# Kernel optimization log

Measured on AMD Instinct MI355X. Metric: run time of the kernel, lower is better.

## Reference

```python
import jax, jax.numpy as jnp
import numpy as np

NODE = 100   # sensors per graph
BATCH = 64
DIM = 128    # embed dim == gnn out channels
IN_DIM = 5
TOPK = 30
INTER = 256  # out_layer hidden
EPS = 1e-5   # BatchNorm eps
SLOPE = 0.2  # leaky relu negative slope


def setup_inputs() -> dict:
    key = jax.random.key(0)
    ks = jax.random.split(key, 16)
    d = {
        "x": jax.random.normal(ks[0], (BATCH * NODE, IN_DIM), jnp.float32),
        "emb": jax.random.normal(ks[1], (NODE, DIM), jnp.float32) * 0.1,
        "w_lin": jax.random.normal(ks[2], (DIM, IN_DIM), jnp.float32) * (1.0 / np.sqrt(IN_DIM)),
        "att_i": jax.random.normal(ks[3], (DIM,), jnp.float32) * (1.0 / np.sqrt(DIM)),
        "att_j": jax.random.normal(ks[4], (DIM,), jnp.float32) * (1.0 / np.sqrt(DIM)),
        "att_em_i": jax.random.normal(ks[5], (DIM,), jnp.float32) * (1.0 / np.sqrt(DIM)),
        "att_em_j": jax.random.normal(ks[6], (DIM,), jnp.float32) * (1.0 / np.sqrt(DIM)),
        "g_bias": jax.random.normal(ks[7], (DIM,), jnp.float32) * 0.02,
        "bn1_g": jnp.ones((DIM,), jnp.float32),
        "bn1_b": jnp.zeros((DIM,), jnp.float32),
        "bn2_g": jnp.ones((DIM,), jnp.float32),
        "bn2_b": jnp.zeros((DIM,), jnp.float32),
        "bn3_g": jnp.ones((INTER,), jnp.float32),
        "bn3_b": jnp.zeros((INTER,), jnp.float32),
        "w1": jax.random.normal(ks[8], (INTER, DIM), jnp.float32) * (1.0 / np.sqrt(DIM)),
        "b1": jnp.zeros((INTER,), jnp.float32),
        "w2": jax.random.normal(ks[9], (1, INTER), jnp.float32) * (1.0 / np.sqrt(INTER)),
        "b2": jnp.zeros((1,), jnp.float32),
        "topk": TOPK,
    }
    return d


def _bn(z, g, b, axes):
    # BatchNorm1d in training mode: biased batch stats per channel (last axis)
    mu = z.mean(axes, keepdims=True)
    var = z.var(axes, keepdims=True)
    return (z - mu) / jnp.sqrt(var + EPS) * g + b


def reference(x, emb, w_lin, att_i, att_j, att_em_i, att_em_j, g_bias,
              bn1_g, bn1_b, bn2_g, bn2_b, bn3_g, bn3_b, w1, b1, w2, b2, topk):
    n, d = emb.shape
    nb = x.shape[0]            # batch*node rows
    bsz = nb // n

    # --- learned graph from cosine similarity of (detached) embeddings ---
    w = jax.lax.stop_gradient(emb)
    nrm = jnp.linalg.norm(w, axis=-1)
    cos = (w @ w.T) / (nrm[:, None] * nrm[None, :])
    _, idx = jax.lax.top_k(cos, topk)              # [n, k] neighbors j per target i
    src = idx.reshape(-1)                          # gated_j (source)
    dst = jnp.repeat(jnp.arange(n), topk)          # gated_i (target)
    off = (jnp.arange(bsz) * n)[:, None]
    src_b = (src[None, :] + off).reshape(-1)       # [bsz*n*k]
    dst_b = (dst[None, :] + off).reshape(-1)

    # --- GraphLayer: lin + gather + edge attention + segment softmax + scatter-add ---
    h = x @ w_lin.T                                # [nb, d]
    x_i = h[dst_b]
    x_j = h[src_b]
    emb_i = emb[dst_b % n]                         # all_embeddings repeated per batch
    emb_j = emb[src_b % n]
    alpha = x_i @ att_i + emb_i @ att_em_i + x_j @ att_j + emb_j @ att_em_j  # [E]
    alpha = jnp.where(alpha > 0, alpha, SLOPE * alpha)
    # segment softmax keyed by target node
    m = jax.ops.segment_max(alpha, dst_b, num_segments=nb)
    a = jnp.exp(alpha - m[dst_b])
    s = jax.ops.segment_sum(a, dst_b, num_segments=nb)
    attw = a / (s[dst_b] + 1e-16)
    agg = jax.ops.segment_sum(x_j * attw[:, None], dst_b, num_segments=nb) + g_bias

    # GNNLayer: BN + ReLU
    y = jax.nn.relu(_bn(agg, bn1_g, bn1_b, 0))     # [nb, d]

    # --- GDN head ---
    x3 = y.reshape(bsz, n, d) * emb[None]          # mul with node embeddings
    x3 = jax.nn.relu(_bn(x3, bn2_g, bn2_b, (0, 1)))
    # OutLayer: Linear -> BN -> ReLU -> Linear
    o = x3 @ w1.T + b1                             # [bsz, n, INTER]
    o = jax.nn.relu(_bn(o, bn3_g, bn3_b, (0, 1)))
    o = o @ w2.T + b2                              # [bsz, n, 1]
    return o.reshape(-1, 1)
```

## Files before the change

### kernel.cpp

```cpp
#include <hip/hip_runtime.h>

#define NODE 100
#define BATCH 64
#define DIM 128
#define IN_DIM 5
#define TOPK 30
#define INTER 256
#define NB (BATCH*NODE)
#define EPS 1e-5f
#define SLOPE 0.2f

__global__ __launch_bounds__(128) void k_lin_att(
        const float* __restrict__ x, const float* __restrict__ emb,
        const float* __restrict__ w_lin,
        const float* __restrict__ att_i, const float* __restrict__ att_j,
        const float* __restrict__ att_em_i, const float* __restrict__ att_em_j,
        float* __restrict__ h, float* __restrict__ ai, float* __restrict__ aj) {
    int row = blockIdx.x;
    int d = threadIdx.x;
    int node = row % NODE;
    float xv[IN_DIM];
#pragma unroll
    for (int c = 0; c < IN_DIM; ++c) xv[c] = x[row*IN_DIM + c];
    float hv = 0.f;
#pragma unroll
    for (int c = 0; c < IN_DIM; ++c) hv += xv[c] * w_lin[d*IN_DIM + c];
    h[row*DIM + d] = hv;
    float e = emb[node*DIM + d];
    float si = hv*att_i[d] + e*att_em_i[d];
    float sj = hv*att_j[d] + e*att_em_j[d];
    __shared__ float s1[DIM], s2[DIM];
    s1[d] = si; s2[d] = sj;
    __syncthreads();
    for (int off = 64; off > 0; off >>= 1) {
        if (d < off) { s1[d] += s1[d+off]; s2[d] += s2[d+off]; }
        __syncthreads();
    }
    if (d == 0) { ai[row] = s1[0]; aj[row] = s2[0]; }
}

__global__ __launch_bounds__(128) void k_topk(const float* __restrict__ emb,
                                              int* __restrict__ idx) {
    int i = blockIdx.x;
    int t = threadIdx.x;
    __shared__ float ei[DIM];
    __shared__ float cosv[NODE];
    __shared__ float rv[128];
    __shared__ int   ri[128];
    ei[t] = emb[i*DIM + t];
    __syncthreads();
    float ni = 0.f;
#pragma unroll
    for (int dd = 0; dd < DIM; ++dd) ni += ei[dd]*ei[dd];
    if (t < NODE) {
        float s = 0.f, nj = 0.f;
        for (int dd = 0; dd < DIM; ++dd) {
            float e = emb[t*DIM + dd];
            s += ei[dd]*e;
            nj += e*e;
        }
        cosv[t] = s / (sqrtf(ni) * sqrtf(nj));
    }
    __syncthreads();
    for (int r = 0; r < TOPK; ++r) {
        float v = (t < NODE) ? cosv[t] : -INFINITY;
        rv[t] = v; ri[t] = t;
        __syncthreads();
        for (int off = 64; off > 0; off >>= 1) {
            if (t < off) {
                float v2 = rv[t+off]; int i2 = ri[t+off];
                if (v2 > rv[t] || (v2 == rv[t] && i2 < ri[t])) { rv[t] = v2; ri[t] = i2; }
            }
            __syncthreads();
        }
        if (t == 0) {
            idx[i*TOPK + r] = ri[0];
            cosv[ri[0]] = -INFINITY;
        }
        __syncthreads();
    }
}

__global__ __launch_bounds__(128) void k_attagg(
        const float* __restrict__ h, const float* __restrict__ ai,
        const float* __restrict__ aj, const int* __restrict__ idx,
        const float* __restrict__ g_bias, float* __restrict__ agg) {
    int tgt = blockIdx.x;
    int t = threadIdx.x;
    int node = tgt % NODE;
    int base = (tgt / NODE) * NODE;
    __shared__ float w[TOPK];
    __shared__ int   srcs[TOPK];
    if (t < TOPK) {
        int s = base + idx[node*TOPK + t];
        srcs[t] = s;
        float a = ai[tgt] + aj[s];
        a = (a > 0.f) ? a : SLOPE*a;
        w[t] = a;
    }
    __syncthreads();
    if (t == 0) {
        float m = -INFINITY;
        for (int r = 0; r < TOPK; ++r) m = fmaxf(m, w[r]);
        float s = 0.f;
        for (int r = 0; r < TOPK; ++r) { float e = expf(w[r]-m); w[r] = e; s += e; }
        float inv = 1.f/(s + 1e-16f);
        for (int r = 0; r < TOPK; ++r) w[r] *= inv;
    }
    __syncthreads();
    float acc = 0.f;
#pragma unroll 5
    for (int r = 0; r < TOPK; ++r) {
        acc += w[r] * h[srcs[r]*DIM + t];
    }
    agg[tgt*DIM + t] = acc + g_bias[t];
}

__global__ __launch_bounds__(256) void k_stats(const float* __restrict__ src, int C,
                                               float* __restrict__ mu,
                                               float* __restrict__ rs) {
    int c = blockIdx.x;
    int t = threadIdx.x;
    float s = 0.f, s2 = 0.f;
    for (int r = t; r < NB; r += 256) {
        float v = src[r*C + c];
        s += v; s2 += v*v;
    }
    __shared__ float a1[256], a2[256];
    a1[t] = s; a2[t] = s2;
    __syncthreads();
    for (int off = 128; off > 0; off >>= 1) {
        if (t < off) { a1[t] += a1[t+off]; a2[t] += a2[t+off]; }
        __syncthreads();
    }
    if (t == 0) {
        float m = a1[0] / (float)NB;
        float var = a2[0]/(float)NB - m*m;
        mu[c] = m;
        rs[c] = rsqrtf(var + EPS);
    }
}

__global__ __launch_bounds__(256) void k_x3(
        const float* __restrict__ agg, const float* __restrict__ emb,
        const float* __restrict__ mu1, const float* __restrict__ rs1,
        const float* __restrict__ g1, const float* __restrict__ b1,
        float* __restrict__ x3) {
    int i = blockIdx.x*256 + threadIdx.x;
    if (i >= NB*DIM) return;
    int d = i & (DIM-1);
    int row = i >> 7;
    int node = row % NODE;
    float v = (agg[i] - mu1[d]) * rs1[d] * g1[d] + b1[d];
    v = fmaxf(v, 0.f);
    x3[i] = v * emb[node*DIM + d];
}

__global__ __launch_bounds__(256) void k_gemm1(
        const float* __restrict__ x3,
        const float* __restrict__ mu2, const float* __restrict__ rs2,
        const float* __restrict__ g2, const float* __restrict__ b2v,
        const float* __restrict__ w1, const float* __restrict__ b1v,
        float* __restrict__ o1) {
    __shared__ float aT[32][36];
    __shared__ float wT[32][260];
    int tid = threadIdx.x;
    int r0 = blockIdx.x * 32;
    int cg = tid & 63;
    int rg = tid >> 6;
    float acc[8][4];
#pragma unroll
    for (int a = 0; a < 8; ++a)
#pragma unroll
        for (int b = 0; b < 4; ++b) acc[a][b] = 0.f;

    for (int k0 = 0; k0 < DIM; k0 += 32) {
#pragma unroll
        for (int j = 0; j < 4; ++j) {
            int i = tid + j*256;
            int kk = i & 31, row = i >> 5;
            int k = k0 + kk;
            float v = (x3[(r0+row)*DIM + k] - mu2[k]) * rs2[k] * g2[k] + b2v[k];
            aT[row][kk] = fmaxf(v, 0.f);
        }
#pragma unroll
        for (int j = 0; j < 32; ++j) {
            int i = tid + j*256;
            int kk = i & 31, c = i >> 5;
            wT[kk][c] = w1[c*DIM + k0 + kk];
        }
        __syncthreads();
#pragma unroll
        for (int q4 = 0; q4 < 8; ++q4) {
            float4 av[8], wv[4];
#pragma unroll
            for (int rr = 0; rr < 8; ++rr)
                av[rr] = *(const float4*)&aT[rg*8+rr][q4*4];
#pragma unroll
            for (int q = 0; q < 4; ++q)
                wv[q] = *(const float4*)&wT[q4*4+q][cg*4];
#pragma unroll
            for (int rr = 0; rr < 8; ++rr) {
                acc[rr][0] += av[rr].x*wv[0].x + av[rr].y*wv[1].x + av[rr].z*wv[2].x + av[rr].w*wv[3].x;
                acc[rr][1] += av[rr].x*wv[0].y + av[rr].y*wv[1].y + av[rr].z*wv[2].y + av[rr].w*wv[3].y;
                acc[rr][2] += av[rr].x*wv[0].z + av[rr].y*wv[1].z + av[rr].z*wv[2].z + av[rr].w*wv[3].z;
                acc[rr][3] += av[rr].x*wv[0].w + av[rr].y*wv[1].w + av[rr].z*wv[2].w + av[rr].w*wv[3].w;
            }
        }
        __syncthreads();
    }
    int cbase = cg*4;
    float4 bv = *(const float4*)&b1v[cbase];
#pragma unroll
    for (int rr = 0; rr < 8; ++rr) {
        int row = r0 + rg*8 + rr;
        float4 o;
        o.x = acc[rr][0] + bv.x;
        o.y = acc[rr][1] + bv.y;
        o.z = acc[rr][2] + bv.z;
        o.w = acc[rr][3] + bv.w;
        *(float4*)&o1[row*INTER + cbase] = o;
    }
}

__global__ __launch_bounds__(256) void k_out(
        const float* __restrict__ o1,
        const float* __restrict__ mu3, const float* __restrict__ rs3,
        const float* __restrict__ g3, const float* __restrict__ b3,
        const float* __restrict__ w2, const float* __restrict__ b2s,
        float* __restrict__ out) {
    int row = blockIdx.x;
    int c = threadIdx.x;
    float v = (o1[row*INTER + c] - mu3[c]) * rs3[c] * g3[c] + b3[c];
    v = fmaxf(v, 0.f);
    v *= w2[c];
    __shared__ float red[256];
    red[c] = v;
    __syncthreads();
    for (int off = 128; off > 0; off >>= 1) {
        if (c < off) red[c] += red[c+off];
        __syncthreads();
    }
    if (c == 0) out[row] = red[0] + b2s[0];
}

extern "C" void kernel_launch(void* const* d_in, const int* in_sizes, int n_in,
                              void* d_out, int out_size, void* d_ws, size_t ws_size,
                              hipStream_t stream) {
    const float* x        = (const float*)d_in[0];
    const float* emb      = (const float*)d_in[1];
    const float* w_lin    = (const float*)d_in[2];
    const float* att_i    = (const float*)d_in[3];
    const float* att_j    = (const float*)d_in[4];
    const float* att_em_i = (const float*)d_in[5];
    const float* att_em_j = (const float*)d_in[6];
    const float* g_bias   = (const float*)d_in[7];
    const float* bn1_g    = (const float*)d_in[8];
    const float* bn1_b    = (const float*)d_in[9];
    const float* bn2_g    = (const float*)d_in[10];
    const float* bn2_b    = (const float*)d_in[11];
    const float* bn3_g    = (const float*)d_in[12];
    const float* bn3_b    = (const float*)d_in[13];
    const float* w1       = (const float*)d_in[14];
    const float* b1       = (const float*)d_in[15];
    const float* w2       = (const float*)d_in[16];
    const float* b2       = (const float*)d_in[17];
    float* out = (float*)d_out;

    float* ws  = (float*)d_ws;
    float* h   = ws;
    float* agg = ws + 819200;
    float* x3  = ws + 1638400;
    float* o1  = ws + 2457600;
    float* ai  = ws + 4096000;
    float* aj  = ws + 4102400;
    float* mu1 = ws + 4108800;
    float* rs1 = mu1 + 128;
    float* mu2 = rs1 + 128;
    float* rs2 = mu2 + 128;
    float* mu3 = rs2 + 128;
    float* rs3 = mu3 + 256;
    int*   idx = (int*)(ws + 4110000);

    k_lin_att<<<NB, 128, 0, stream>>>(x, emb, w_lin, att_i, att_j, att_em_i,
                                      att_em_j, h, ai, aj);
    k_topk<<<NODE, 128, 0, stream>>>(emb, idx);
    k_attagg<<<NB, 128, 0, stream>>>(h, ai, aj, idx, g_bias, agg);
    k_stats<<<DIM, 256, 0, stream>>>(agg, DIM, mu1, rs1);
    k_x3<<<(NB*DIM + 255)/256, 256, 0, stream>>>(agg, emb, mu1, rs1, bn1_g, bn1_b, x3);
    k_stats<<<DIM, 256, 0, stream>>>(x3, DIM, mu2, rs2);
    k_gemm1<<<NB/32, 256, 0, stream>>>(x3, mu2, rs2, bn2_g, bn2_b, w1, b1, o1);
    k_stats<<<INTER, 256, 0, stream>>>(o1, INTER, mu3, rs3);
    k_out<<<NB, 256, 0, stream>>>(o1, mu3, rs3, bn3_g, bn3_b, w2, b2, out);
}
```

Measured before the change: 201.9 us.

## Fuse BN statistics into producers via atomics and use wave-level reductions

New measurement: 223.3 us. +10.6%, slower.

```diff
diff --git a/kernel.cpp b/kernel.cpp
--- a/kernel.cpp
+++ b/kernel.cpp
@@ -10,184 +10,206 @@
 #define EPS 1e-5f
 #define SLOPE 0.2f
 
-__global__ __launch_bounds__(128) void k_lin_att(
+#define LIN_BLOCKS 1600
+#define TOPK_BLOCKS 25
+#define ZERO_BLOCK (LIN_BLOCKS + TOPK_BLOCKS)
+#define FRONT_GRID (ZERO_BLOCK + 1)
+
+
+__global__ __launch_bounds__(256) void k_front(
         const float* __restrict__ x, const float* __restrict__ emb,
         const float* __restrict__ w_lin,
         const float* __restrict__ att_i, const float* __restrict__ att_j,
         const float* __restrict__ att_em_i, const float* __restrict__ att_em_j,
-        float* __restrict__ h, float* __restrict__ ai, float* __restrict__ aj) {
-    int row = blockIdx.x;
-    int d = threadIdx.x;
-    int node = row % NODE;
-    float xv[IN_DIM];
-#pragma unroll
-    for (int c = 0; c < IN_DIM; ++c) xv[c] = x[row*IN_DIM + c];
-    float hv = 0.f;
-#pragma unroll
-    for (int c = 0; c < IN_DIM; ++c) hv += xv[c] * w_lin[d*IN_DIM + c];
-    h[row*DIM + d] = hv;
-    float e = emb[node*DIM + d];
-    float si = hv*att_i[d] + e*att_em_i[d];
-    float sj = hv*att_j[d] + e*att_em_j[d];
-    __shared__ float s1[DIM], s2[DIM];
-    s1[d] = si; s2[d] = sj;
-    __syncthreads();
-    for (int off = 64; off > 0; off >>= 1) {
-        if (d < off) { s1[d] += s1[d+off]; s2[d] += s2[d+off]; }
+        float* __restrict__ h, float* __restrict__ ai, float* __restrict__ aj,
+        int* __restrict__ idx, float* __restrict__ stats) {
+    int b = blockIdx.x;
+    int t = threadIdx.x;
+    int w = t >> 6;
+    int l = t & 63;
+    if (b < LIN_BLOCKS) {
+        int row = b*4 + w;
+        int node = row % NODE;
+        float xv[IN_DIM];
+#pragma unroll
+        for (int c = 0; c < IN_DIM; ++c) xv[c] = x[row*IN_DIM + c];
+        float h0 = 0.f, h1 = 0.f;
+#pragma unroll
+        for (int c = 0; c < IN_DIM; ++c) {
+            h0 += xv[c] * w_lin[l*IN_DIM + c];
+            h1 += xv[c] * w_lin[(l+64)*IN_DIM + c];
+        }
+        h[row*DIM + l]      = h0;
+        h[row*DIM + l + 64] = h1;
+        float e0 = emb[node*DIM + l], e1 = emb[node*DIM + l + 64];
+        float si = h0*att_i[l] + e0*att_em_i[l] + h1*att_i[l+64] + e1*att_em_i[l+64];
+        float sj = h0*att_j[l] + e0*att_em_j[l] + h1*att_j[l+64] + e1*att_em_j[l+64];
+#pragma unroll
+        for (int m = 32; m >= 1; m >>= 1) {
+            si += __shfl_xor(si, m, 64);
+            sj += __shfl_xor(sj, m, 64);
+        }
+        if (l == 0) { ai[row] = si; aj[row] = sj; }
+    } else if (b < ZERO_BLOCK) {
+        __shared__ float eis[4][DIM];
+        int i = (b - LIN_BLOCKS)*4 + w;
+        eis[w][l]      = emb[i*DIM + l];
+        eis[w][l + 64] = emb[i*DIM + l + 64];
         __syncthreads();
-    }
-    if (d == 0) { ai[row] = s1[0]; aj[row] = s2[0]; }
-}
-
-__global__ __launch_bounds__(128) void k_topk(const float* __restrict__ emb,
-                                              int* __restrict__ idx) {
-    int i = blockIdx.x;
-    int t = threadIdx.x;
-    __shared__ float ei[DIM];
-    __shared__ float cosv[NODE];
-    __shared__ float rv[128];
-    __shared__ int   ri[128];
-    ei[t] = emb[i*DIM + t];
-    __syncthreads();
-    float ni = 0.f;
-#pragma unroll
-    for (int dd = 0; dd < DIM; ++dd) ni += ei[dd]*ei[dd];
-    if (t < NODE) {
-        float s = 0.f, nj = 0.f;
+        int j0 = l, j1 = 64 + l;
+        bool v1ok = (j1 < NODE);
+        float d0 = 0.f, d1 = 0.f, ni = 0.f, n0 = 0.f, n1 = 0.f;
         for (int dd = 0; dd < DIM; ++dd) {
-            float e = emb[t*DIM + dd];
-            s += ei[dd]*e;
-            nj += e*e;
-        }
-        cosv[t] = s / (sqrtf(ni) * sqrtf(nj));
-    }
-    __syncthreads();
-    for (int r = 0; r < TOPK; ++r) {
-        float v = (t < NODE) ? cosv[t] : -INFINITY;
-        rv[t] = v; ri[t] = t;
-        __syncthreads();
-        for (int off = 64; off > 0; off >>= 1) {
-            if (t < off) {
-                float v2 = rv[t+off]; int i2 = ri[t+off];
-                if (v2 > rv[t] || (v2 == rv[t] && i2 < ri[t])) { rv[t] = v2; ri[t] = i2; }
+            float e = eis[w][dd];
+            ni += e*e;
+            float a0 = emb[j0*DIM + dd];
+            d0 += e*a0; n0 += a0*a0;
+            if (v1ok) { float a1 = emb[j1*DIM + dd]; d1 += e*a1; n1 += a1*a1; }
+        }
+        float sni = sqrtf(ni);
+        float c0 = d0 / (sni * sqrtf(n0));
+        float c1 = v1ok ? d1 / (sni * sqrtf(n1)) : -INFINITY;
+        for (int r = 0; r < TOPK; ++r) {
+            float bv; int bi;
+            if (c1 > c0) { bv = c1; bi = j1; } else { bv = c0; bi = j0; }
+#pragma unroll
+            for (int m = 32; m >= 1; m >>= 1) {
+                float ov = __shfl_xor(bv, m, 64);
+                int   oi = __shfl_xor(bi, m, 64);
+                if (ov > bv || (ov == bv && oi < bi)) { bv = ov; bi = oi; }
             }
-            __syncthreads();
-        }
-        if (t == 0) {
-            idx[i*TOPK + r] = ri[0];
-            cosv[ri[0]] = -INFINITY;
-        }
-        __syncthreads();
-    }
-}
-
-__global__ __launch_bounds__(128) void k_attagg(
+            if (l == 0) idx[i*TOPK + r] = bi;
+            if (bi == j0) c0 = -INFINITY;
+            if (bi == j1) c1 = -INFINITY;
+        }
+    } else {
+#pragma unroll
+        for (int q = 0; q < 4; ++q) stats[t + q*256] = 0.f;
+    }
+}
+
+__global__ __launch_bounds__(256) void k_attagg(
         const float* __restrict__ h, const float* __restrict__ ai,
         const float* __restrict__ aj, const int* __restrict__ idx,
-        const float* __restrict__ g_bias, float* __restrict__ agg) {
-    int tgt = blockIdx.x;
-    int t = threadIdx.x;
+        const float* __restrict__ g_bias, float* __restrict__ agg,
+        float* __restrict__ stats) {
+    __shared__ float sv[4][DIM], sq[4][DIM];
+    int t = threadIdx.x, w = t >> 6, l = t & 63;
+    int tgt = blockIdx.x*4 + w;
     int node = tgt % NODE;
-    int base = (tgt / NODE) * NODE;
-    __shared__ float w[TOPK];
-    __shared__ int   srcs[TOPK];
-    if (t < TOPK) {
-        int s = base + idx[node*TOPK + t];
-        srcs[t] = s;
-        float a = ai[tgt] + aj[s];
-        a = (a > 0.f) ? a : SLOPE*a;
-        w[t] = a;
-    }
+    int base = tgt - node;
+    float a = -INFINITY; int s = 0;
+    if (l < TOPK) {
+        s = base + idx[node*TOPK + l];
+        float v = ai[tgt] + aj[s];
+        a = (v > 0.f) ? v : SLOPE*v;
+    }
+    float m = a;
+#pragma unroll
+    for (int mm = 32; mm >= 1; mm >>= 1) m = fmaxf(m, __shfl_xor(m, mm, 64));
+    float e = (l < TOPK) ? expf(a - m) : 0.f;
+    float sum = e;
+#pragma unroll
+    for (int mm = 32; mm >= 1; mm >>= 1) sum += __shfl_xor(sum, mm, 64);
+    float wgt = e / (sum + 1e-16f);
+    float acc0 = 0.f, acc1 = 0.f;
+#pragma unroll 10
+    for (int r = 0; r < TOPK; ++r) {
+        float wr = __shfl(wgt, r, 64);
+        int   sr = __shfl(s,   r, 64);
+        acc0 += wr * h[sr*DIM + l];
+        acc1 += wr * h[sr*DIM + l + 64];
+    }
+    float v0 = acc0 + g_bias[l];
+    float v1 = acc1 + g_bias[l + 64];
+    agg[tgt*DIM + l]      = v0;
+    agg[tgt*DIM + l + 64] = v1;
+    sv[w][l] = v0;      sv[w][l+64] = v1;
+    sq[w][l] = v0*v0;   sq[w][l+64] = v1*v1;
     __syncthreads();
-    if (t == 0) {
-        float m = -INFINITY;
-        for (int r = 0; r < TOPK; ++r) m = fmaxf(m, w[r]);
-        float s = 0.f;
-        for (int r = 0; r < TOPK; ++r) { float e = expf(w[r]-m); w[r] = e; s += e; }
-        float inv = 1.f/(s + 1e-16f);
-        for (int r = 0; r < TOPK; ++r) w[r] *= inv;
-    }
-    __syncthreads();
-    float acc = 0.f;
-#pragma unroll 5
-    for (int r = 0; r < TOPK; ++r) {
-        acc += w[r] * h[srcs[r]*DIM + t];
-    }
-    agg[tgt*DIM + t] = acc + g_bias[t];
-}
-
-__global__ __launch_bounds__(256) void k_stats(const float* __restrict__ src, int C,
-                                               float* __restrict__ mu,
-                                               float* __restrict__ rs) {
-    int c = blockIdx.x;
-    int t = threadIdx.x;
-    float s = 0.f, s2 = 0.f;
-    for (int r = t; r < NB; r += 256) {
-        float v = src[r*C + c];
-        s += v; s2 += v*v;
-    }
-    __shared__ float a1[256], a2[256];
-    a1[t] = s; a2[t] = s2;
-    __syncthreads();
-    for (int off = 128; off > 0; off >>= 1) {
-        if (t < off) { a1[t] += a1[t+off]; a2[t] += a2[t+off]; }
-        __syncthreads();
-    }
-    if (t == 0) {
-        float m = a1[0] / (float)NB;
-        float var = a2[0]/(float)NB - m*m;
-        mu[c] = m;
-        rs[c] = rsqrtf(var + EPS);
+    if (t < DIM) {
+        float s1 = sv[0][t] + sv[1][t] + sv[2][t] + sv[3][t];
+        float s2 = sq[0][t] + sq[1][t] + sq[2][t] + sq[3][t];
+        atomicAdd(&stats[t], s1);
+        atomicAdd(&stats[DIM + t], s2);
     }
 }
 
 __global__ __launch_bounds__(256) void k_x3(
         const float* __restrict__ agg, const float* __restrict__ emb,
-        const float* __restrict__ mu1, const float* __restrict__ rs1,
         const float* __restrict__ g1, const float* __restrict__ b1,
-        float* __restrict__ x3) {
-    int i = blockIdx.x*256 + threadIdx.x;
-    if (i >= NB*DIM) return;
-    int d = i & (DIM-1);
-    int row = i >> 7;
+        float* __restrict__ stats, float* __restrict__ x3) {
+    __shared__ float pv[8][DIM], pq[8][DIM];
+    int t = threadIdx.x;
+    int i4 = blockIdx.x*256 + t;
+    int c4 = (i4 & 31) * 4;
+    int row = i4 >> 5;
     int node = row % NODE;
-    float v = (agg[i] - mu1[d]) * rs1[d] * g1[d] + b1[d];
-    v = fmaxf(v, 0.f);
-    x3[i] = v * emb[node*DIM + d];
+    float4 av = ((const float4*)agg)[i4];
+    float4 ev = *(const float4*)&emb[node*DIM + c4];
+    const float inv = 1.f/(float)NB;
+    float o[4];
+#pragma unroll
+    for (int q = 0; q < 4; ++q) {
+        int c = c4 + q;
+        float mu = stats[c] * inv;
+        float var = stats[DIM + c]*inv - mu*mu;
+        float rs = rsqrtf(var + EPS);
+        float val = (((const float*)&av)[q] - mu)*rs*g1[c] + b1[c];
+        val = fmaxf(val, 0.f);
+        o[q] = val * ((const float*)&ev)[q];
+    }
+    ((float4*)x3)[i4] = make_float4(o[0], o[1], o[2], o[3]);
+    int lr = t >> 5;
+    *(float4*)&pv[lr][c4] = make_float4(o[0], o[1], o[2], o[3]);
+    *(float4*)&pq[lr][c4] = make_float4(o[0]*o[0], o[1]*o[1], o[2]*o[2], o[3]*o[3]);
+    __syncthreads();
+    if (t < DIM) {
+        float s1 = 0.f, s2 = 0.f;
+#pragma unroll
+        for (int r = 0; r < 8; ++r) { s1 += pv[r][t]; s2 += pq[r][t]; }
+        atomicAdd(&stats[2*DIM + t], s1);
+        atomicAdd(&stats[3*DIM + t], s2);
+    }
 }
 
 __global__ __launch_bounds__(256) void k_gemm1(
         const float* __restrict__ x3,
-        const float* __restrict__ mu2, const float* __restrict__ rs2,
         const float* __restrict__ g2, const float* __restrict__ b2v,
         const float* __restrict__ w1, const float* __restrict__ b1v,
-        float* __restrict__ o1) {
+        float* __restrict__ stats, float* __restrict__ o1) {
     __shared__ float aT[32][36];
     __shared__ float wT[32][260];
+    __shared__ float ps[4][INTER], ps2[4][INTER];
     int tid = threadIdx.x;
     int r0 = blockIdx.x * 32;
     int cg = tid & 63;
     int rg = tid >> 6;
+    const float inv = 1.f/(float)NB;
     float acc[8][4];
 #pragma unroll
     for (int a = 0; a < 8; ++a)
 #pragma unroll
         for (int b = 0; b < 4; ++b) acc[a][b] = 0.f;
 
+    int kk = tid & 31;
     for (int k0 = 0; k0 < DIM; k0 += 32) {
+        int k = k0 + kk;
+        float mu = stats[2*DIM + k] * inv;
+        float var = stats[3*DIM + k]*inv - mu*mu;
+        float rs = rsqrtf(var + EPS);
+        float gg = g2[k], bb = b2v[k];
 #pragma unroll
         for (int j = 0; j < 4; ++j) {
-            int i = tid + j*256;
-            int kk = i & 31, row = i >> 5;
-            int k = k0 + kk;
-            float v = (x3[(r0+row)*DIM + k] - mu2[k]) * rs2[k] * g2[k] + b2v[k];
+            int row = (tid >> 5) + j*8;
+            float v = (x3[(r0+row)*DIM + k] - mu)*rs*gg + bb;
             aT[row][kk] = fmaxf(v, 0.f);
         }
 #pragma unroll
         for (int j = 0; j < 32; ++j) {
             int i = tid + j*256;
-            int kk = i & 31, c = i >> 5;
-            wT[kk][c] = w1[c*DIM + k0 + kk];
+            int kk2 = i & 31, c = i >> 5;
+            wT[kk2][c] = w1[c*DIM + k0 + kk2];
         }
         __syncthreads();
 #pragma unroll
@@ -211,37 +233,55 @@
     }
     int cbase = cg*4;
     float4 bv = *(const float4*)&b1v[cbase];
+    float lv[4]  = {0.f, 0.f, 0.f, 0.f};
+    float lv2[4] = {0.f, 0.f, 0.f, 0.f};
 #pragma unroll
     for (int rr = 0; rr < 8; ++rr) {
         int row = r0 + rg*8 + rr;
-        float4 o;
-        o.x = acc[rr][0] + bv.x;
-        o.y = acc[rr][1] + bv.y;
-        o.z = acc[rr][2] + bv.z;
-        o.w = acc[rr][3] + bv.w;
-        *(float4*)&o1[row*INTER + cbase] = o;
+        float o0 = acc[rr][0] + bv.x;
+        float o1v = acc[rr][1] + bv.y;
+        float o2 = acc[rr][2] + bv.z;
+        float o3 = acc[rr][3] + bv.w;
+        *(float4*)&o1[row*INTER + cbase] = make_float4(o0, o1v, o2, o3);
+        lv[0] += o0;  lv2[0] += o0*o0;
+        lv[1] += o1v; lv2[1] += o1v*o1v;
+        lv[2] += o2;  lv2[2] += o2*o2;
+        lv[3] += o3;  lv2[3] += o3*o3;
+    }
+    *(float4*)&ps[rg][cbase]  = make_float4(lv[0], lv[1], lv[2], lv[3]);
+    *(float4*)&ps2[rg][cbase] = make_float4(lv2[0], lv2[1], lv2[2], lv2[3]);
+    __syncthreads();
+    if (tid < INTER) {
+        float s1 = ps[0][tid] + ps[1][tid] + ps[2][tid] + ps[3][tid];
+        float s2 = ps2[0][tid] + ps2[1][tid] + ps2[2][tid] + ps2[3][tid];
+        atomicAdd(&stats[4*DIM + tid], s1);
+        atomicAdd(&stats[4*DIM + INTER + tid], s2);
     }
 }
 
 __global__ __launch_bounds__(256) void k_out(
-        const float* __restrict__ o1,
-        const float* __restrict__ mu3, const float* __restrict__ rs3,
+        const float* __restrict__ o1, const float* __restrict__ stats,
         const float* __restrict__ g3, const float* __restrict__ b3,
         const float* __restrict__ w2, const float* __restrict__ b2s,
         float* __restrict__ out) {
-    int row = blockIdx.x;
-    int c = threadIdx.x;
-    float v = (o1[row*INTER + c] - mu3[c]) * rs3[c] * g3[c] + b3[c];
-    v = fmaxf(v, 0.f);
-    v *= w2[c];
-    __shared__ float red[256];
-    red[c] = v;
-    __syncthreads();
-    for (int off = 128; off > 0; off >>= 1) {
-        if (c < off) red[c] += red[c+off];
-        __syncthreads();
-    }
-    if (c == 0) out[row] = red[0] + b2s[0];
+    int t = threadIdx.x, w = t >> 6, l = t & 63;
+    int row = blockIdx.x*4 + w;
+    const float inv = 1.f/(float)NB;
+    float4 v = *(const float4*)&o1[row*INTER + l*4];
+    float s = 0.f;
+#pragma unroll
+    for (int q = 0; q < 4; ++q) {
+        int c = l*4 + q;
+        float mu = stats[4*DIM + c]*inv;
+        float var = stats[4*DIM + INTER + c]*inv - mu*mu;
+        float rs = rsqrtf(var + EPS);
+        float val = (((const float*)&v)[q] - mu)*rs*g3[c] + b3[c];
+        val = fmaxf(val, 0.f);
+        s += val * w2[c];
+    }
+#pragma unroll
+    for (int m = 32; m >= 1; m >>= 1) s += __shfl_xor(s, m, 64);
+    if (l == 0) out[row] = s + b2s[0];
 }
 
 extern "C" void kernel_launch(void* const* d_in, const int* in_sizes, int n_in,
@@ -267,29 +307,20 @@
     const float* b2       = (const float*)d_in[17];
     float* out = (float*)d_out;
 
-    float* ws  = (float*)d_ws;
-    float* h   = ws;
-    float* agg = ws + 819200;
-    float* x3  = ws + 1638400;
-    float* o1  = ws + 2457600;
-    float* ai  = ws + 4096000;
-    float* aj  = ws + 4102400;
-    float* mu1 = ws + 4108800;
-    float* rs1 = mu1 + 128;
-    float* mu2 = rs1 + 128;
-    float* rs2 = mu2 + 128;
-    float* mu3 = rs2 + 128;
-    float* rs3 = mu3 + 256;
-    int*   idx = (int*)(ws + 4110000);
-
-    k_lin_att<<<NB, 128, 0, stream>>>(x, emb, w_lin, att_i, att_j, att_em_i,
-                                      att_em_j, h, ai, aj);
-    k_topk<<<NODE, 128, 0, stream>>>(emb, idx);
-    k_attagg<<<NB, 128, 0, stream>>>(h, ai, aj, idx, g_bias, agg);
-    k_stats<<<DIM, 256, 0, stream>>>(agg, DIM, mu1, rs1);
-    k_x3<<<(NB*DIM + 255)/256, 256, 0, stream>>>(agg, emb, mu1, rs1, bn1_g, bn1_b, x3);
-    k_stats<<<DIM, 256, 0, stream>>>(x3, DIM, mu2, rs2);
-    k_gemm1<<<NB/32, 256, 0, stream>>>(x3, mu2, rs2, bn2_g, bn2_b, w1, b1, o1);
-    k_stats<<<INTER, 256, 0, stream>>>(o1, INTER, mu3, rs3);
-    k_out<<<NB, 256, 0, stream>>>(o1, mu3, rs3, bn3_g, bn3_b, w2, b2, out);
-}
+    float* ws    = (float*)d_ws;
+    float* h     = ws;
+    float* agg   = ws + 819200;
+    float* x3    = ws + 1638400;
+    float* o1    = ws + 2457600;
+    float* ai    = ws + 4096000;
+    float* aj    = ws + 4102400;
+    float* stats = ws + 4108800;
+    int*   idx   = (int*)(ws + 4110000);
+
+    k_front<<<FRONT_GRID, 256, 0, stream>>>(x, emb, w_lin, att_i, att_j,
+                                            att_em_i, att_em_j, h, ai, aj, idx, stats);
+    k_attagg<<<NB/4, 256, 0, stream>>>(h, ai, aj, idx, g_bias, agg, stats);
+    k_x3<<<NB*DIM/4/256, 256, 0, stream>>>(agg, emb, bn1_g, bn1_b, stats, x3);
+    k_gemm1<<<NB/32, 256, 0, stream>>>(x3, bn2_g, bn2_b, w1, b1, stats, o1);
+    k_out<<<NB/4, 256, 0, stream>>>(o1, stats, bn3_g, bn3_b, w2, b2, out);
+}
```
